# Kernel optimization log

Measured on AMD Instinct MI355X. Metric: run time of the kernel, lower is better.

Reference implementation:

```python
import jax, jax.numpy as jnp
import numpy as np

EPS = 1e-5

def layernorm(x, w, b):
    mu = x.mean(-1, keepdims=True)
    var = x.var(-1, keepdims=True)
    return (x - mu) / jnp.sqrt(var + EPS) * w + b

def silu(x):
    return x * jax.nn.sigmoid(x)

def causal_dwconv(x, w, b):
    # x: (B,L,D), w: (D,K) depthwise causal conv along L
    K = w.shape[1]
    xt = jnp.moveaxis(x, 1, 2)                      # (B,D,L)
    xt = jnp.pad(xt, ((0, 0), (0, 0), (K - 1, 0)))
    y = jax.lax.conv_general_dilated(xt, w[:, None, :], (1,), 'VALID',
        dimension_numbers=('NCH', 'OIH', 'NCH'), feature_group_count=w.shape[0])
    return jnp.moveaxis(y + b[None, :, None], 2, 1)

def mamba_layer(x, p):
    # LayerNorm + Mamba selective scan; returns (out, C) with C the per-step C projection ("C_fast")
    xn = layernorm(x, p['ln_w'], p['ln_b'])
    xz = xn @ p['in_proj_w']                        # (B,L,2*Di)
    Di = p['conv_w'].shape[0]
    xh, z = xz[..., :Di], xz[..., Di:]
    xh = silu(causal_dwconv(xh, p['conv_w'], p['conv_b']))
    dbl = xh @ p['x_proj_w']                        # (B,L,R+2*S)
    R = p['dt_proj_w'].shape[0]
    S = p['A_log'].shape[1]
    dt = jax.nn.softplus(dbl[..., :R] @ p['dt_proj_w'] + p['dt_proj_b'])  # (B,L,Di)
    Bm = dbl[..., R:R + S]                          # (B,L,S)
    Cm = dbl[..., R + S:]                           # (B,L,S)
    A = -jnp.exp(p['A_log'])                        # (Di,S)
    dA = jnp.exp(dt[..., None] * A)                 # (B,L,Di,S)
    dBx = dt[..., None] * Bm[:, :, None, :] * xh[..., None]
    def step(h, inp):
        a, bx = inp
        h = a * h + bx
        return h, h
    h0 = jnp.zeros((x.shape[0], Di, S), x.dtype)
    _, hs = jax.lax.scan(step, h0, (jnp.moveaxis(dA, 1, 0), jnp.moveaxis(dBx, 1, 0)))
    y = jnp.einsum('lbds,bls->bld', hs, Cm) + p['D'] * xh
    y = y * silu(z)
    return y @ p['out_proj_w'], Cm

def run_chunks(x, k, p):
    # contiguous L-chunks folded into batch (chunks are independent sequences)
    B, L, D = x.shape
    y, C = mamba_layer(x.reshape(B * k, L // k, D), p)
    return y.reshape(B, L, D), C.reshape(B, k, L // k, -1)

def batchnorm(h, g, b):
    mu = h.mean((0, 1))
    var = h.var((0, 1))
    return (h - mu) / jnp.sqrt(var + EPS) * g + b

def freq_ffn(x, fc1_w, bn1_g, bn1_b, r_mat, i_mat, rb, ib, fc2_w, bn2_g, bn2_b):
    h = jax.nn.relu(batchnorm(jnp.einsum('bnc,hc->bnh', x, fc1_w), bn1_g, bn1_b))
    xf = jnp.fft.fft(h, axis=1, norm='ortho')
    # torch einsum 'bnc,cc->bnc' multiplies by the DIAGONAL of the matrix
    rd = jnp.diagonal(r_mat)
    idg = jnp.diagonal(i_mat)
    xr = jax.nn.relu(xf.real * rd - xf.imag * idg + rb)
    xi = jax.nn.relu(xf.imag * rd + xf.real * idg + ib)
    h = jnp.fft.ifft(xr + 1j * xi, axis=1, norm='ortho').real.astype(x.dtype)
    return batchnorm(jnp.einsum('bnh,ch->bnc', h, fc2_w), bn2_g, bn2_b)


def setup_inputs() -> dict:
    key = jax.random.key(0)
    B, L, D = 4, 512, 128
    Di, S, R, K, H = 256, 64, 8, 4, 256
    ks = jax.random.split(key, 16)
    rn = lambda k, sh, s=1.0: (jax.random.normal(k, sh) * s).astype(jnp.float32)
    return {
        'x': rn(ks[0], (B, L, D)),
        'ln_w': jnp.ones((D,), jnp.float32), 'ln_b': jnp.zeros((D,), jnp.float32),
        'in_proj_w': rn(ks[1], (D, 2 * Di), D ** -0.5),
        'conv_w': rn(ks[2], (Di, K), 0.3),
        'conv_b': jnp.zeros((Di,), jnp.float32),
        'x_proj_w': rn(ks[3], (Di, R + 2 * S), Di ** -0.5),
        'dt_proj_w': rn(ks[4], (R, Di), R ** -0.5),
        'dt_proj_b': rn(ks[5], (Di,), 0.1) - 4.0,
        'A_log': jnp.log(jnp.tile(jnp.arange(1, S + 1, dtype=jnp.float32), (Di, 1))),
        'D_param': jnp.ones((Di,), jnp.float32),
        'out_proj_w': rn(ks[6], (Di, D), Di ** -0.5),
        'norm1_w': jnp.ones((D,), jnp.float32), 'norm1_b': jnp.zeros((D,), jnp.float32),
        'norm2_w': jnp.ones((D,), jnp.float32), 'norm2_b': jnp.zeros((D,), jnp.float32),
        'fc1_w': rn(ks[7], (H, D), D ** -0.5),
        'bn1_g': jnp.ones((H,), jnp.float32), 'bn1_b': jnp.zeros((H,), jnp.float32),
        'r_mat': rn(ks[8], (H, H), 0.02),
        'i_mat': rn(ks[9], (H, H), 0.02),
        'rb': rn(ks[10], (H,), 0.02),
        'ib': rn(ks[11], (H,), 0.02),
        'fc2_w': rn(ks[12], (D, H), H ** -0.5),
        'bn2_g': jnp.ones((D,), jnp.float32), 'bn2_b': jnp.zeros((D,), jnp.float32),
    }


def reference(x, ln_w, ln_b, in_proj_w, conv_w, conv_b, x_proj_w, dt_proj_w, dt_proj_b,
              A_log, D_param, out_proj_w, norm1_w, norm1_b, norm2_w, norm2_b,
              fc1_w, bn1_g, bn1_b, r_mat, i_mat, rb, ib, fc2_w, bn2_g, bn2_b):
    p = dict(ln_w=ln_w, ln_b=ln_b, in_proj_w=in_proj_w, conv_w=conv_w, conv_b=conv_b,
             x_proj_w=x_proj_w, dt_proj_w=dt_proj_w, dt_proj_b=dt_proj_b,
             A_log=A_log, D=D_param, out_proj_w=out_proj_w)
    x_o, C0 = mamba_layer(x, p)                 # full sequence
    y1, C1 = run_chunks(x, 2, p)                # 2 halves
    y2, C2 = run_chunks(x, 4, p)                # 4 quarters
    y3, C3 = run_chunks(x, 8, p)                # 8 eighths
    x_o = x_o + y1 + y2 + y3                    # drop_path = Identity
    xo = x + layernorm(x_o, norm1_w, norm1_b)
    out = xo + freq_ffn(layernorm(xo, norm2_w, norm2_b),
                        fc1_w, bn1_g, bn1_b, r_mat, i_mat, rb, ib, fc2_w, bn2_g, bn2_b)
    return out, C0, C1, C2, C3
```

## Files before the change

### kernel.cpp

```cpp
#include <hip/hip_runtime.h>
#include <hip/hip_bf16.h>
#include <math.h>


constexpr int NT = 2048;
constexpr int Di = 256;
constexpr float EPSF = 1e-5f;
constexpr float LOG2E = 1.4426950408889634f;
constexpr float ISQ512 = 0.04419417382415922f;

typedef __attribute__((ext_vector_type(8))) short short8;
typedef __attribute__((ext_vector_type(4))) float f32x4;

constexpr long O_CS2B  = 0;
constexpr long O_CSIB  = 262144;
constexpr long O_A2    = 524288;
constexpr long O_FC1B  = 540672;
constexpr long O_FC2B  = 557056;
constexpr long O_INPB  = 573440;
constexpr long O_XPB   = 606208;
constexpr long O_OPB   = 630784;
constexpr long O_RD    = 647168;
constexpr long O_IDG   = 647424;
constexpr long O_XNB   = 647680;
constexpr long O_XZ    = 778752;
constexpr long O_XH    = 1827328;
constexpr long O_DBL   = 3924480;
constexpr long O_DTT   = 5038592;
constexpr long O_YS    = 7135744;
constexpr long O_XO    = 9232896;
constexpr long O_LN2B  = 9495040;
constexpr long O_H1    = 9626112;
constexpr long O_H1NTB = 10150400;
constexpr long O_XRI   = 10412544;
constexpr long O_XRITB = 11461120;
constexpr long O_H2B   = 11985408;
constexpr long O_F2    = 12247552;
constexpr long O_ST1   = 12509696;
constexpr long O_ST2   = 12510208;
constexpr long O_DXT   = O_H1;
constexpr long O_XHB   = O_H1;
constexpr long O_YACCB = O_F2;
constexpr long O_XO1   = O_H2B;

__device__ __forceinline__ ushort bf16bits(float v) {
  __hip_bfloat16 h = __float2bfloat16(v);
  return *(ushort*)&h;
}

__global__ __launch_bounds__(256) void k_tables(
    const float* __restrict__ A_log, const float* __restrict__ fc1_w,
    const float* __restrict__ fc2_w, const float* __restrict__ r_mat,
    const float* __restrict__ i_mat, const float* __restrict__ in_proj_w,
    const float* __restrict__ x_proj_w, const float* __restrict__ out_proj_w,
    float* __restrict__ ws) {
  __shared__ float ct[512];
  int tid = threadIdx.x;
  ct[tid]       = cosf((float)tid * (6.283185307179586f / 512.0f)) * ISQ512;
  ct[tid + 256] = cosf((float)(tid + 256) * (6.283185307179586f / 512.0f)) * ISQ512;
  __syncthreads();
  __hip_bfloat16* cs2b = (__hip_bfloat16*)(ws + O_CS2B);
  __hip_bfloat16* csib = (__hip_bfloat16*)(ws + O_CSIB);
  int i = blockIdx.x * 256 + tid;
  if (i < 524288) {
    int r = i >> 9, n = i & 511;
    float v;
    if (r < 512) v = ct[(r * n) & 511];
    else         v = -ct[((r - 512) * n + 384) & 511];
    cs2b[i] = __float2bfloat16(v);
  } else {
    int j = i - 524288;
    int n = j >> 10, kp = j & 1023;
    float v;
    if (kp < 512) v = ct[(n * kp) & 511];
    else          v = -ct[(n * (kp - 512) + 384) & 511];
    csib[j] = __float2bfloat16(v);
  }
  if (i < 16384) ws[O_A2 + i] = -expf(A_log[i]) * LOG2E;
  if (i < 32768) {
    ((__hip_bfloat16*)(ws + O_FC1B))[i] = __float2bfloat16(fc1_w[i]);
    ((__hip_bfloat16*)(ws + O_FC2B))[i] = __float2bfloat16(fc2_w[i]);
  }
  if (i < 65536) {
    int n = i >> 7, k = i & 127;
    ((__hip_bfloat16*)(ws + O_INPB))[i] = __float2bfloat16(in_proj_w[k * 512 + n]);
  }
  if (i < 49152) {
    int n = i >> 8, k = i & 255;
    float v = (n < 136) ? x_proj_w[k * 136 + n] : 0.f;
    ((__hip_bfloat16*)(ws + O_XPB))[i] = __float2bfloat16(v);
  }
  if (i < 32768 + 0) {}
  if (i >= 65536 && i < 65536 + 32768) {
    int j = i - 65536;
    int n = j >> 8, k = j & 255;
    ((__hip_bfloat16*)(ws + O_OPB))[j] = __float2bfloat16(out_proj_w[k * 128 + n]);
  }
  if (i < 256) {
    ws[O_RD + i] = r_mat[i * 256 + i];
    ws[O_IDG + i] = i_mat[i * 256 + i];
  }
}

__global__ void k_ln1(const float* __restrict__ x, const float* __restrict__ w,
                      const float* __restrict__ b, ushort* __restrict__ outb) {
  int lane = threadIdx.x & 63;
  int t = (blockIdx.x * 256 + threadIdx.x) >> 6;
  float v0 = x[t * 128 + lane], v1 = x[t * 128 + 64 + lane];
  float s = v0 + v1, sq = v0 * v0 + v1 * v1;
#pragma unroll
  for (int off = 32; off; off >>= 1) { s += __shfl_xor(s, off); sq += __shfl_xor(sq, off); }
  float mu = s * (1.f / 128.f);
  float rstd = rsqrtf(sq * (1.f / 128.f) - mu * mu + EPSF);
  outb[t * 128 + lane]      = bf16bits((v0 - mu) * rstd * w[lane] + b[lane]);
  outb[t * 128 + 64 + lane] = bf16bits((v1 - mu) * rstd * w[64 + lane] + b[64 + lane]);
}

__global__ void k_lndbl(const float* __restrict__ x, const float* __restrict__ xo1,
                        const float* __restrict__ w1, const float* __restrict__ b1,
                        const float* __restrict__ w2, const float* __restrict__ b2,
                        float* __restrict__ xo, ushort* __restrict__ ln2b) {
  int lane = threadIdx.x & 63;
  int t = (blockIdx.x * 256 + threadIdx.x) >> 6;
  float u0 = xo1[t * 128 + lane], u1 = xo1[t * 128 + 64 + lane];
  float s = u0 + u1, sq = u0 * u0 + u1 * u1;
#pragma unroll
  for (int off = 32; off; off >>= 1) { s += __shfl_xor(s, off); sq += __shfl_xor(sq, off); }
  float mu = s * (1.f / 128.f);
  float rstd = rsqrtf(sq * (1.f / 128.f) - mu * mu + EPSF);
  float a0 = x[t * 128 + lane]      + (u0 - mu) * rstd * w1[lane] + b1[lane];
  float a1 = x[t * 128 + 64 + lane] + (u1 - mu) * rstd * w1[64 + lane] + b1[64 + lane];
  xo[t * 128 + lane] = a0;
  xo[t * 128 + 64 + lane] = a1;
  s = a0 + a1; sq = a0 * a0 + a1 * a1;
#pragma unroll
  for (int off = 32; off; off >>= 1) { s += __shfl_xor(s, off); sq += __shfl_xor(sq, off); }
  mu = s * (1.f / 128.f);
  rstd = rsqrtf(sq * (1.f / 128.f) - mu * mu + EPSF);
  ln2b[t * 128 + lane]      = bf16bits((a0 - mu) * rstd * w2[lane] + b2[lane]);
  ln2b[t * 128 + 64 + lane] = bf16bits((a1 - mu) * rstd * w2[64 + lane] + b2[64 + lane]);
}

template <bool OUTBF16>
__global__ __launch_bounds__(256) void k_gmfma(const ushort* __restrict__ A,
                                               const ushort* __restrict__ Bt,
                                               void* __restrict__ Cv,
                                               int M, int N, int K,
                                               long sA, long sBt, long sC) {
  A += (long)blockIdx.z * sA;
  Bt += (long)blockIdx.z * sBt;
  int lane = threadIdx.x & 63, wid = threadIdx.x >> 6;
  int m0 = blockIdx.y * 64 + wid * 16, n0 = blockIdx.x * 64;
  const ushort* arow = A + (long)(m0 + (lane & 15)) * K + (lane >> 4) * 8;
  const ushort* brow = Bt + (long)(n0 + (lane & 15)) * K + (lane >> 4) * 8;
  f32x4 acc0 = {0.f, 0.f, 0.f, 0.f}, acc1 = acc0, acc2 = acc0, acc3 = acc0;
#pragma unroll 4
  for (int k0 = 0; k0 < K; k0 += 32) {
    short8 av = *(const short8*)(arow + k0);
    short8 b0 = *(const short8*)(brow + k0);
    short8 b1 = *(const short8*)(brow + 16L * K + k0);
    short8 b2 = *(const short8*)(brow + 32L * K + k0);
    short8 b3 = *(const short8*)(brow + 48L * K + k0);
    acc0 = __builtin_amdgcn_mfma_f32_16x16x32_bf16(av, b0, acc0, 0, 0, 0);
    acc1 = __builtin_amdgcn_mfma_f32_16x16x32_bf16(av, b1, acc1, 0, 0, 0);
    acc2 = __builtin_amdgcn_mfma_f32_16x16x32_bf16(av, b2, acc2, 0, 0, 0);
    acc3 = __builtin_amdgcn_mfma_f32_16x16x32_bf16(av, b3, acc3, 0, 0, 0);
  }
  int r0 = (lane >> 4) * 4, c0 = lane & 15;
#pragma unroll
  for (int j = 0; j < 4; ++j) {
    long row = m0 + r0 + j;
    float v[4] = {acc0[j], acc1[j], acc2[j], acc3[j]};
    if (OUTBF16) {
      __hip_bfloat16* C = (__hip_bfloat16*)Cv + blockIdx.z * sC;
#pragma unroll
      for (int c = 0; c < 4; ++c) {
        int n = n0 + c * 16 + c0;
        if (n < N) C[row * N + n] = __float2bfloat16(v[c]);
      }
    } else {
      float* C = (float*)Cv + blockIdx.z * sC;
#pragma unroll
      for (int c = 0; c < 4; ++c) {
        int n = n0 + c * 16 + c0;
        if (n < N) C[row * N + n] = v[c];
      }
    }
  }
}

__global__ void k_conv4(const float* __restrict__ xz, const float* __restrict__ cw,
                        const float* __restrict__ cb, float* __restrict__ xh,
                        ushort* __restrict__ xhb) {
  int i = blockIdx.x * 256 + threadIdx.x;
  int t = i >> 8, d = i & 255;
  float w0 = cw[d * 4 + 0], w1 = cw[d * 4 + 1], w2 = cw[d * 4 + 2], w3 = cw[d * 4 + 3];
  float bias = cb[d];
  float x0  = xz[(long)t * 512 + d];
  float xm1 = t >= 1 ? xz[(long)(t - 1) * 512 + d] : 0.f;
  float xm2 = t >= 2 ? xz[(long)(t - 2) * 512 + d] : 0.f;
  float xm3 = t >= 3 ? xz[(long)(t - 3) * 512 + d] : 0.f;
  if ((t & 63) >= 3) {
    float s = fmaf(w0, xm3, fmaf(w1, xm2, fmaf(w2, xm1, fmaf(w3, x0, bias))));
    float sil = s / (1.f + expf(-s));
    ushort sb = bf16bits(sil);
#pragma unroll
    for (int v = 0; v < 4; ++v) { xh[v * 524288 + i] = sil; xhb[v * 524288 + i] = sb; }
  } else {
#pragma unroll
    for (int v = 0; v < 4; ++v) {
      int lv = t & ((512 >> v) - 1);
      float s = fmaf(w3, x0, bias);
      if (lv >= 1) s = fmaf(w2, xm1, s);
      if (lv >= 2) s = fmaf(w1, xm2, s);
      if (lv >= 3) s = fmaf(w0, xm3, s);
      float sil = s / (1.f + expf(-s));
      xh[v * 524288 + i] = sil;
      xhb[v * 524288 + i] = bf16bits(sil);
    }
  }
}

__global__ __launch_bounds__(256) void k_dtx(const float* __restrict__ dbl,
                                             const float* __restrict__ xh,
                                             const float* __restrict__ w,
                                             const float* __restrict__ bias,
                                             float* __restrict__ DTT,
                                             float* __restrict__ DXT,
                                             float* __restrict__ outC) {
  __shared__ float r8T[8][64];
  __shared__ float xt[64][65];
  __shared__ float wt[8][64];
  int v = blockIdx.z, t0 = blockIdx.y * 64, d0 = blockIdx.x * 64;
  int j = threadIdx.x;
  if (j < 128) {
    int t = j >> 1, half = j & 1;
    float4 q = *(const float4*)&dbl[((long)v * NT + t0 + t) * 136 + half * 4];
    r8T[half * 4 + 0][t] = q.x; r8T[half * 4 + 1][t] = q.y;
    r8T[half * 4 + 2][t] = q.z; r8T[half * 4 + 3][t] = q.w;
  } else {
    int idx = j - 128;
    int r = idx >> 4, dl4 = (idx & 15) * 4;
    float4 q = *(const float4*)&w[r * 256 + d0 + dl4];
    wt[r][dl4] = q.x; wt[r][dl4 + 1] = q.y; wt[r][dl4 + 2] = q.z; wt[r][dl4 + 3] = q.w;
  }
#pragma unroll
  for (int it = 0; it < 4; ++it) {
    int row = (j >> 4) + it * 16, col4 = (j & 15) * 4;
    float4 q = *(const float4*)&xh[((long)v * NT + t0 + row) * 256 + d0 + col4];
    xt[row][col4] = q.x; xt[row][col4 + 1] = q.y;
    xt[row][col4 + 2] = q.z; xt[row][col4 + 3] = q.w;
  }
  __syncthreads();
  int lane = j & 63, w4 = j >> 6;
#pragma unroll
  for (int k = 0; k < 16; ++k) {
    int dl = w4 * 16 + k, d = d0 + dl;
    float s = bias[d];
#pragma unroll
    for (int r = 0; r < 8; ++r) s = fmaf(r8T[r][lane], wt[r][dl], s);
    float dtv = fmaxf(s, 0.f) + log1pf(expf(-fabsf(s)));
    float dx = dtv * xt[lane][dl];
    long oi = ((long)(v * 256 + d)) * 2048 + t0 + lane;
    DTT[oi] = dtv;
    DXT[oi] = dx;
  }
  if (blockIdx.x == 0) {
#pragma unroll
    for (int k2 = 0; k2 < 16; ++k2) {
      int idx = k2 * 256 + j;
      int tl = idx >> 6, s2 = idx & 63;
      outC[(long)v * 131072 + (long)(t0 + tl) * 64 + s2] =
          dbl[((long)v * NT + t0 + tl) * 136 + 72 + s2];
    }
  }
}

template <int CTRL>
__device__ __forceinline__ float dpp_add(float x) {
  int t = __builtin_amdgcn_update_dpp(0, __float_as_int(x), CTRL, 0xF, 0xF, true);
  return x + __int_as_float(t);
}

__global__ __launch_bounds__(256) void k_scan(const float* __restrict__ DTT,
                                              const float* __restrict__ DXT,
                                              const float* __restrict__ dbl,
                                              const float* __restrict__ A2,
                                              float* __restrict__ ys) {
  int lane = threadIdx.x & 63;
  int gwid = (blockIdx.x * 256 + threadIdx.x) >> 6;
  int v, base;
  if (gwid < 1024)      { v = 0; base = 0; }
  else if (gwid < 3072) { v = 1; base = 1024; }
  else if (gwid < 7168) { v = 2; base = 3072; }
  else                  { v = 3; base = 7168; }
  int local = gwid - base;
  int b = local >> 8, d = local & 255;
  int Lp = 512 >> v;
  int t0 = b * Lp;
  const float* dtrow = DTT + ((long)(v * 256 + d)) * 2048 + t0;
  const float* dxrow = DXT + ((long)(v * 256 + d)) * 2048 + t0;
  const float* dblp = dbl + ((long)v * NT + t0) * 136;
  float* ysp = ys + (long)v * NT * Di + (long)((b << 8) + d) * Lp;
  float a2 = A2[d * 64 + lane];
  float h = 0.f;

#define LOADG(BB, CC, G)                                                     \
  _Pragma("unroll") for (int q = 0; q < 8; ++q) {                            \
    BB[q] = rowp[((G) * 8 + q) * 136 + 8 + lane];                            \
    CC[q] = rowp[((G) * 8 + q) * 136 + 72 + lane];                           \
  }
#define PROCG(BB, CC, G)                                                     \
  _Pragma("unroll") for (int q = 0; q < 8; ++q) {                            \
    int l2 = (G) * 8 + q;                                                    \
    float sdt = __int_as_float(__builtin_amdgcn_readlane(__float_as_int(rdt), l2)); \
    float sdx = __int_as_float(__builtin_amdgcn_readlane(__float_as_int(rdx), l2)); \
    float a = __builtin_amdgcn_exp2f(sdt * a2);                              \
    h = fmaf(a, h, sdx * BB[q]);                                             \
    float p = h * CC[q];                                                     \
    p = dpp_add<0x111>(p); p = dpp_add<0x112>(p);                            \
    p = dpp_add<0x114>(p); p = dpp_add<0x118>(p);                            \
    p = dpp_add<0x142>(p); p = dpp_add<0x143>(p);                            \
    float tot = __int_as_float(__builtin_amdgcn_readlane(__float_as_int(p), 63)); \
    if (lane == l2) ybuf = tot;                                              \
  }

  for (int c = 0; c < Lp; c += 64) {
    float rdt = dtrow[c + lane];
    float rdx = dxrow[c + lane];
    const float* rowp = dblp + (long)c * 136;
    float ybuf = 0.f;
    float b0[8], c0[8], b1[8], c1[8];
    LOADG(b0, c0, 0)
    LOADG(b1, c1, 1)
    PROCG(b0, c0, 0) LOADG(b0, c0, 2)
    PROCG(b1, c1, 1) LOADG(b1, c1, 3)
    PROCG(b0, c0, 2) LOADG(b0, c0, 4)
    PROCG(b1, c1, 3) LOADG(b1, c1, 5)
    PROCG(b0, c0, 4) LOADG(b0, c0, 6)
    PROCG(b1, c1, 5) LOADG(b1, c1, 7)
    PROCG(b0, c0, 6)
    PROCG(b1, c1, 7)
    ysp[c + lane] = ybuf;
  }
#undef LOADG
#undef PROCG
}

__global__ void k_yfull(const float* __restrict__ ys, const float* __restrict__ xh,
                        const float* __restrict__ xz, const float* __restrict__ Dp,
                        ushort* __restrict__ yaccb) {
  int i = blockIdx.x * 256 + threadIdx.x;
  int t = i >> 8, d = i & 255;
  float z = xz[(long)t * 512 + 256 + d];
  float sil = z / (1.f + expf(-z));
  float Dd = Dp[d];
  float s = 0.f;
#pragma unroll
  for (int v = 0; v < 4; ++v) {
    int Lp = 512 >> v;
    int b = t >> (9 - v);
    int l = t & (Lp - 1);
    float ysv = ys[(long)v * NT * Di + (long)((b << 8) + d) * Lp + l];
    float xhv = xh[(long)v * NT * Di + i];
    s += ysv + Dd * xhv;
  }
  yaccb[i] = bf16bits(s * sil);
}

__global__ __launch_bounds__(256) void k_bnstats(const float* __restrict__ h, int F,
                                                 const float* __restrict__ g,
                                                 const float* __restrict__ b,
                                                 float* __restrict__ scale,
                                                 float* __restrict__ shift) {
  int f = blockIdx.x;
  float s = 0.f, sq = 0.f;
  for (int t = threadIdx.x; t < NT; t += 256) {
    float v = h[(long)t * F + f];
    s += v; sq += v * v;
  }
#pragma unroll
  for (int off = 32; off; off >>= 1) { s += __shfl_xor(s, off); sq += __shfl_xor(sq, off); }
  __shared__ float red[2][4];
  int w = threadIdx.x >> 6;
  if ((threadIdx.x & 63) == 0) { red[0][w] = s; red[1][w] = sq; }
  __syncthreads();
  if (threadIdx.x == 0) {
    s = red[0][0] + red[0][1] + red[0][2] + red[0][3];
    sq = red[1][0] + red[1][1] + red[1][2] + red[1][3];
    float mu = s * (1.f / NT);
    float var = sq * (1.f / NT) - mu * mu;
    float sc = g[f] * rsqrtf(var + EPSF);
    scale[f] = sc;
    shift[f] = b[f] - mu * sc;
  }
}

__global__ __launch_bounds__(256) void k_bnreluT(const float* __restrict__ h1,
                                                 const float* __restrict__ scale,
                                                 const float* __restrict__ shift,
                                                 ushort* __restrict__ outT) {
  __shared__ float tile[64][65];
  int t0 = blockIdx.x * 64, f0 = blockIdx.y * 64, b = blockIdx.z;
  int tid = threadIdx.x;
#pragma unroll
  for (int i = 0; i < 16; ++i) {
    int idx = i * 256 + tid;
    int r = idx >> 6, c = idx & 63;
    int f = f0 + c;
    float v = h1[((long)(b * 512 + t0 + r)) * 256 + f];
    tile[r][c] = fmaxf(fmaf(v, scale[f], shift[f]), 0.f);
  }
  __syncthreads();
  int tc2 = (tid & 31) * 2, fr0 = tid >> 5;
#pragma unroll
  for (int i = 0; i < 8; ++i) {
    int fr = fr0 + i * 8;
    uint u = ((uint)bf16bits(tile[tc2 + 1][fr]) << 16) | bf16bits(tile[tc2][fr]);
    long off = (long)b * 131072 + (long)(f0 + fr) * 512 + t0 + tc2;
    *(uint*)(outT + off) = u;
  }
}

__global__ __launch_bounds__(256) void k_freqT(const float* __restrict__ XRI,
                                               const float* __restrict__ rd,
                                               const float* __restrict__ idg,
                                               const float* __restrict__ rb,
                                               const float* __restrict__ ib,
                                               ushort* __restrict__ outT) {
  __shared__ float tr[64][65], ti[64][65];
  int n0 = blockIdx.x * 64, f0 = blockIdx.y * 64, b = blockIdx.z;
  int tid = threadIdx.x;
#pragma unroll
  for (int i = 0; i < 16; ++i) {
    int idx = i * 256 + tid;
    int r = idx >> 6, c = idx & 63;
    int f = f0 + c;
    long base = (long)b * 262144 + (long)(n0 + r) * 256 + f;
    float a = XRI[base], b2 = XRI[base + 131072];
    tr[r][c] = fmaxf(a * rd[f] - b2 * idg[f] + rb[f], 0.f);
    ti[r][c] = fmaxf(b2 * rd[f] + a * idg[f] + ib[f], 0.f);
  }
  __syncthreads();
  int tc2 = (tid & 31) * 2, fr0 = tid >> 5;
#pragma unroll
  for (int i = 0; i < 8; ++i) {
    int fr = fr0 + i * 8;
    long offr = (long)b * 262144 + (long)(f0 + fr) * 1024 + n0 + tc2;
    uint ur = ((uint)bf16bits(tr[tc2 + 1][fr]) << 16) | bf16bits(tr[tc2][fr]);
    uint ui = ((uint)bf16bits(ti[tc2 + 1][fr]) << 16) | bf16bits(ti[tc2][fr]);
    *(uint*)(outT + offr) = ur;
    *(uint*)(outT + offr + 512) = ui;
  }
}

__global__ void k_final(const float* __restrict__ xo, const float* __restrict__ f2,
                        const float* __restrict__ scale, const float* __restrict__ shift,
                        float* __restrict__ out) {
  int i = blockIdx.x * 256 + threadIdx.x;
  int c = i & 127;
  out[i] = xo[i] + fmaf(f2[i], scale[c], shift[c]);
}

extern "C" void kernel_launch(void* const* d_in, const int* in_sizes, int n_in,
                              void* d_out, int out_size, void* d_ws, size_t ws_size,
                              hipStream_t stream) {
  const float* x         = (const float*)d_in[0];
  const float* ln_w      = (const float*)d_in[1];
  const float* ln_b      = (const float*)d_in[2];
  const float* in_proj_w = (const float*)d_in[3];
  const float* conv_w    = (const float*)d_in[4];
  const float* conv_b    = (const float*)d_in[5];
  const float* x_proj_w  = (const float*)d_in[6];
  const float* dt_proj_w = (const float*)d_in[7];
  const float* dt_proj_b = (const float*)d_in[8];
  const float* A_log     = (const float*)d_in[9];
  const float* D_param   = (const float*)d_in[10];
  const float* out_proj_w= (const float*)d_in[11];
  const float* n1w       = (const float*)d_in[12];
  const float* n1b       = (const float*)d_in[13];
  const float* n2w       = (const float*)d_in[14];
  const float* n2b       = (const float*)d_in[15];
  const float* fc1_w     = (const float*)d_in[16];
  const float* bn1_g     = (const float*)d_in[17];
  const float* bn1_b     = (const float*)d_in[18];
  const float* r_mat     = (const float*)d_in[19];
  const float* i_mat     = (const float*)d_in[20];
  const float* rb        = (const float*)d_in[21];
  const float* ib        = (const float*)d_in[22];
  const float* fc2_w     = (const float*)d_in[23];
  const float* bn2_g     = (const float*)d_in[24];
  const float* bn2_b     = (const float*)d_in[25];
  float* ws  = (float*)d_ws;
  float* out = (float*)d_out;

  k_tables<<<4096, 256, 0, stream>>>(A_log, fc1_w, fc2_w, r_mat, i_mat,
                                     in_proj_w, x_proj_w, out_proj_w, ws);
  k_ln1<<<512, 256, 0, stream>>>(x, ln_w, ln_b, (ushort*)(ws + O_XNB));
  k_gmfma<false><<<dim3(8, 32, 1), 256, 0, stream>>>(
      (const ushort*)(ws + O_XNB), (const ushort*)(ws + O_INPB), ws + O_XZ,
      2048, 512, 128, 0, 0, 0);
  k_conv4<<<2048, 256, 0, stream>>>(ws + O_XZ, conv_w, conv_b, ws + O_XH,
                                    (ushort*)(ws + O_XHB));
  k_gmfma<false><<<dim3(3, 32, 4), 256, 0, stream>>>(
      (const ushort*)(ws + O_XHB), (const ushort*)(ws + O_XPB), ws + O_DBL,
      2048, 136, 256, 524288L, 0, 278528L);
  k_dtx<<<dim3(4, 32, 4), 256, 0, stream>>>(ws + O_DBL, ws + O_XH, dt_proj_w,
                                            dt_proj_b, ws + O_DTT, ws + O_DXT,
                                            out + 262144);
  k_scan<<<3840, 256, 0, stream>>>(ws + O_DTT, ws + O_DXT, ws + O_DBL,
                                   ws + O_A2, ws + O_YS);
  k_yfull<<<2048, 256, 0, stream>>>(ws + O_YS, ws + O_XH, ws + O_XZ, D_param,
                                    (ushort*)(ws + O_YACCB));
  k_gmfma<false><<<dim3(2, 32, 1), 256, 0, stream>>>(
      (const ushort*)(ws + O_YACCB), (const ushort*)(ws + O_OPB), ws + O_XO1,
      2048, 128, 256, 0, 0, 0);
  k_lndbl<<<512, 256, 0, stream>>>(x, ws + O_XO1, n1w, n1b, n2w, n2b,
                                   ws + O_XO, (ushort*)(ws + O_LN2B));
  k_gmfma<false><<<dim3(4, 32, 1), 256, 0, stream>>>(
      (const ushort*)(ws + O_LN2B), (const ushort*)(ws + O_FC1B), ws + O_H1,
      2048, 256, 128, 0, 0, 0);
  k_bnstats<<<256, 256, 0, stream>>>(ws + O_H1, 256, bn1_g, bn1_b,
                                     ws + O_ST1, ws + O_ST1 + 256);
  k_bnreluT<<<dim3(8, 4, 4), 256, 0, stream>>>(ws + O_H1, ws + O_ST1,
                                               ws + O_ST1 + 256,
                                               (ushort*)(ws + O_H1NTB));
  k_gmfma<false><<<dim3(4, 16, 4), 256, 0, stream>>>(
      (const ushort*)(ws + O_CS2B), (const ushort*)(ws + O_H1NTB), ws + O_XRI,
      1024, 256, 512, 0, 131072L, 262144L);
  k_freqT<<<dim3(8, 4, 4), 256, 0, stream>>>(ws + O_XRI, ws + O_RD, ws + O_IDG,
                                             rb, ib, (ushort*)(ws + O_XRITB));
  k_gmfma<true><<<dim3(4, 8, 4), 256, 0, stream>>>(
      (const ushort*)(ws + O_CSIB), (const ushort*)(ws + O_XRITB), ws + O_H2B,
      512, 256, 1024, 0, 262144L, 131072L);
  k_gmfma<false><<<dim3(2, 32, 1), 256, 0, stream>>>(
      (const ushort*)(ws + O_H2B), (const ushort*)(ws + O_FC2B), ws + O_F2,
      2048, 128, 256, 0, 0, 0);
  k_bnstats<<<128, 256, 0, stream>>>(ws + O_F2, 128, bn2_g, bn2_b,
                                     ws + O_ST2, ws + O_ST2 + 128);
  k_final<<<1024, 256, 0, stream>>>(ws + O_XO, ws + O_F2, ws + O_ST2,
                                    ws + O_ST2 + 128, out);
}
```

Measured before the change: 297.5 us.

## Store xz/xh intermediates in bf16, fuse LN1 into tables, atomic BN stats

```diff
diff --git a/kernel.cpp b/kernel.cpp
--- a/kernel.cpp
+++ b/kernel.cpp
@@ -23,8 +23,8 @@
 constexpr long O_RD    = 647168;
 constexpr long O_IDG   = 647424;
 constexpr long O_XNB   = 647680;
-constexpr long O_XZ    = 778752;
-constexpr long O_XH    = 1827328;
+constexpr long O_XZB   = 778752;
+constexpr long O_XHB   = 1827328;
 constexpr long O_DBL   = 3924480;
 constexpr long O_DTT   = 5038592;
 constexpr long O_YS    = 7135744;
@@ -36,16 +36,18 @@
 constexpr long O_XRITB = 11461120;
 constexpr long O_H2B   = 11985408;
 constexpr long O_F2    = 12247552;
-constexpr long O_ST1   = 12509696;
-constexpr long O_ST2   = 12510208;
+constexpr long O_SQ1   = 12509696;
+constexpr long O_SQ2   = 12510208;
 constexpr long O_DXT   = O_H1;
-constexpr long O_XHB   = O_H1;
 constexpr long O_YACCB = O_F2;
 constexpr long O_XO1   = O_H2B;
 
 __device__ __forceinline__ ushort bf16bits(float v) {
   __hip_bfloat16 h = __float2bfloat16(v);
   return *(ushort*)&h;
+}
+__device__ __forceinline__ float bfu(ushort u) {
+  return __uint_as_float((uint)u << 16);
 }
 
 __global__ __launch_bounds__(256) void k_tables(
@@ -53,7 +55,8 @@
     const float* __restrict__ fc2_w, const float* __restrict__ r_mat,
     const float* __restrict__ i_mat, const float* __restrict__ in_proj_w,
     const float* __restrict__ x_proj_w, const float* __restrict__ out_proj_w,
-    float* __restrict__ ws) {
+    const float* __restrict__ x, const float* __restrict__ ln_w,
+    const float* __restrict__ ln_b, float* __restrict__ ws) {
   __shared__ float ct[512];
   int tid = threadIdx.x;
   ct[tid]       = cosf((float)tid * (6.283185307179586f / 512.0f)) * ISQ512;
@@ -90,8 +93,7 @@
     float v = (n < 136) ? x_proj_w[k * 136 + n] : 0.f;
     ((__hip_bfloat16*)(ws + O_XPB))[i] = __float2bfloat16(v);
   }
-  if (i < 32768 + 0) {}
-  if (i >= 65536 && i < 65536 + 32768) {
+  if (i >= 65536 && i < 98304) {
     int j = i - 65536;
     int n = j >> 8, k = j & 255;
     ((__hip_bfloat16*)(ws + O_OPB))[j] = __float2bfloat16(out_proj_w[k * 128 + n]);
@@ -100,20 +102,21 @@
     ws[O_RD + i] = r_mat[i * 256 + i];
     ws[O_IDG + i] = i_mat[i * 256 + i];
   }
-}
-
-__global__ void k_ln1(const float* __restrict__ x, const float* __restrict__ w,
-                      const float* __restrict__ b, ushort* __restrict__ outb) {
-  int lane = threadIdx.x & 63;
-  int t = (blockIdx.x * 256 + threadIdx.x) >> 6;
-  float v0 = x[t * 128 + lane], v1 = x[t * 128 + 64 + lane];
-  float s = v0 + v1, sq = v0 * v0 + v1 * v1;
-#pragma unroll
-  for (int off = 32; off; off >>= 1) { s += __shfl_xor(s, off); sq += __shfl_xor(sq, off); }
-  float mu = s * (1.f / 128.f);
-  float rstd = rsqrtf(sq * (1.f / 128.f) - mu * mu + EPSF);
-  outb[t * 128 + lane]      = bf16bits((v0 - mu) * rstd * w[lane] + b[lane]);
-  outb[t * 128 + 64 + lane] = bf16bits((v1 - mu) * rstd * w[64 + lane] + b[64 + lane]);
+  if (i < 512) ws[O_SQ1 + i] = 0.f;
+  if (i < 256) ws[O_SQ2 + i] = 0.f;
+  if (blockIdx.x < 512) {
+    ushort* outb = (ushort*)(ws + O_XNB);
+    int lane = tid & 63;
+    int t = (blockIdx.x * 256 + tid) >> 6;
+    float v0 = x[t * 128 + lane], v1 = x[t * 128 + 64 + lane];
+    float s = v0 + v1, sq = v0 * v0 + v1 * v1;
+#pragma unroll
+    for (int off = 32; off; off >>= 1) { s += __shfl_xor(s, off); sq += __shfl_xor(sq, off); }
+    float mu = s * (1.f / 128.f);
+    float rstd = rsqrtf(sq * (1.f / 128.f) - mu * mu + EPSF);
+    outb[t * 128 + lane]      = bf16bits((v0 - mu) * rstd * ln_w[lane] + ln_b[lane]);
+    outb[t * 128 + 64 + lane] = bf16bits((v1 - mu) * rstd * ln_w[64 + lane] + ln_b[64 + lane]);
+  }
 }
 
 __global__ void k_lndbl(const float* __restrict__ x, const float* __restrict__ xo1,
@@ -189,23 +192,22 @@
   }
 }
 
-__global__ void k_conv4(const float* __restrict__ xz, const float* __restrict__ cw,
-                        const float* __restrict__ cb, float* __restrict__ xh,
-                        ushort* __restrict__ xhb) {
+__global__ void k_conv4(const ushort* __restrict__ xzb, const float* __restrict__ cw,
+                        const float* __restrict__ cb, ushort* __restrict__ xhb) {
   int i = blockIdx.x * 256 + threadIdx.x;
   int t = i >> 8, d = i & 255;
   float w0 = cw[d * 4 + 0], w1 = cw[d * 4 + 1], w2 = cw[d * 4 + 2], w3 = cw[d * 4 + 3];
   float bias = cb[d];
-  float x0  = xz[(long)t * 512 + d];
-  float xm1 = t >= 1 ? xz[(long)(t - 1) * 512 + d] : 0.f;
-  float xm2 = t >= 2 ? xz[(long)(t - 2) * 512 + d] : 0.f;
-  float xm3 = t >= 3 ? xz[(long)(t - 3) * 512 + d] : 0.f;
+  float x0  = bfu(xzb[(long)t * 512 + d]);
+  float xm1 = t >= 1 ? bfu(xzb[(long)(t - 1) * 512 + d]) : 0.f;
+  float xm2 = t >= 2 ? bfu(xzb[(long)(t - 2) * 512 + d]) : 0.f;
+  float xm3 = t >= 3 ? bfu(xzb[(long)(t - 3) * 512 + d]) : 0.f;
   if ((t & 63) >= 3) {
     float s = fmaf(w0, xm3, fmaf(w1, xm2, fmaf(w2, xm1, fmaf(w3, x0, bias))));
     float sil = s / (1.f + expf(-s));
     ushort sb = bf16bits(sil);
 #pragma unroll
-    for (int v = 0; v < 4; ++v) { xh[v * 524288 + i] = sil; xhb[v * 524288 + i] = sb; }
+    for (int v = 0; v < 4; ++v) xhb[v * 524288 + i] = sb;
   } else {
 #pragma unroll
     for (int v = 0; v < 4; ++v) {
@@ -215,14 +217,13 @@
       if (lv >= 2) s = fmaf(w1, xm2, s);
       if (lv >= 3) s = fmaf(w0, xm3, s);
       float sil = s / (1.f + expf(-s));
-      xh[v * 524288 + i] = sil;
       xhb[v * 524288 + i] = bf16bits(sil);
     }
   }
 }
 
 __global__ __launch_bounds__(256) void k_dtx(const float* __restrict__ dbl,
-                                             const float* __restrict__ xh,
+                                             const ushort* __restrict__ xhb,
                                              const float* __restrict__ w,
                                              const float* __restrict__ bias,
                                              float* __restrict__ DTT,
@@ -247,9 +248,11 @@
 #pragma unroll
   for (int it = 0; it < 4; ++it) {
     int row = (j >> 4) + it * 16, col4 = (j & 15) * 4;
-    float4 q = *(const float4*)&xh[((long)v * NT + t0 + row) * 256 + d0 + col4];
-    xt[row][col4] = q.x; xt[row][col4 + 1] = q.y;
-    xt[row][col4 + 2] = q.z; xt[row][col4 + 3] = q.w;
+    uint2 u = *(const uint2*)&xhb[((long)v * NT + t0 + row) * 256 + d0 + col4];
+    xt[row][col4 + 0] = __uint_as_float(u.x << 16);
+    xt[row][col4 + 1] = __uint_as_float(u.x & 0xffff0000u);
+    xt[row][col4 + 2] = __uint_as_float(u.y << 16);
+    xt[row][col4 + 3] = __uint_as_float(u.y & 0xffff0000u);
   }
   __syncthreads();
   int lane = j & 63, w4 = j >> 6;
@@ -347,12 +350,12 @@
 #undef PROCG
 }
 
-__global__ void k_yfull(const float* __restrict__ ys, const float* __restrict__ xh,
-                        const float* __restrict__ xz, const float* __restrict__ Dp,
+__global__ void k_yfull(const float* __restrict__ ys, const ushort* __restrict__ xhb,
+                        const ushort* __restrict__ xzb, const float* __restrict__ Dp,
                         ushort* __restrict__ yaccb) {
   int i = blockIdx.x * 256 + threadIdx.x;
   int t = i >> 8, d = i & 255;
-  float z = xz[(long)t * 512 + 256 + d];
+  float z = bfu(xzb[(long)t * 512 + 256 + d]);
   float sil = z / (1.f + expf(-z));
   float Dd = Dp[d];
   float s = 0.f;
@@ -362,54 +365,54 @@
     int b = t >> (9 - v);
     int l = t & (Lp - 1);
     float ysv = ys[(long)v * NT * Di + (long)((b << 8) + d) * Lp + l];
-    float xhv = xh[(long)v * NT * Di + i];
+    float xhv = bfu(xhb[(long)v * 524288 + i]);
     s += ysv + Dd * xhv;
   }
   yaccb[i] = bf16bits(s * sil);
 }
 
-__global__ __launch_bounds__(256) void k_bnstats(const float* __restrict__ h, int F,
+template <int F>
+__global__ __launch_bounds__(256) void k_bnpart(const float* __restrict__ h,
+                                                float* __restrict__ SQ) {
+  constexpr int NREP = 256 / F;
+  constexpr int TPR = 32 / NREP;
+  int tid = threadIdx.x;
+  int f = tid & (F - 1), rep = tid / F;
+  int t0 = blockIdx.x * 32 + rep * TPR;
+  float s = 0.f, q = 0.f;
+#pragma unroll
+  for (int tt = 0; tt < TPR; ++tt) {
+    float v = h[(long)(t0 + tt) * F + f];
+    s += v; q += v * v;
+  }
+  atomicAdd(&SQ[f], s);
+  atomicAdd(&SQ[F + f], q);
+}
+
+__global__ __launch_bounds__(256) void k_bnreluT(const float* __restrict__ h1,
+                                                 const float* __restrict__ SQ,
                                                  const float* __restrict__ g,
-                                                 const float* __restrict__ b,
-                                                 float* __restrict__ scale,
-                                                 float* __restrict__ shift) {
-  int f = blockIdx.x;
-  float s = 0.f, sq = 0.f;
-  for (int t = threadIdx.x; t < NT; t += 256) {
-    float v = h[(long)t * F + f];
-    s += v; sq += v * v;
-  }
-#pragma unroll
-  for (int off = 32; off; off >>= 1) { s += __shfl_xor(s, off); sq += __shfl_xor(sq, off); }
-  __shared__ float red[2][4];
-  int w = threadIdx.x >> 6;
-  if ((threadIdx.x & 63) == 0) { red[0][w] = s; red[1][w] = sq; }
-  __syncthreads();
-  if (threadIdx.x == 0) {
-    s = red[0][0] + red[0][1] + red[0][2] + red[0][3];
-    sq = red[1][0] + red[1][1] + red[1][2] + red[1][3];
-    float mu = s * (1.f / NT);
-    float var = sq * (1.f / NT) - mu * mu;
-    float sc = g[f] * rsqrtf(var + EPSF);
-    scale[f] = sc;
-    shift[f] = b[f] - mu * sc;
-  }
-}
-
-__global__ __launch_bounds__(256) void k_bnreluT(const float* __restrict__ h1,
-                                                 const float* __restrict__ scale,
-                                                 const float* __restrict__ shift,
+                                                 const float* __restrict__ bb,
                                                  ushort* __restrict__ outT) {
   __shared__ float tile[64][65];
+  __shared__ float sc_s[64], sh_s[64];
   int t0 = blockIdx.x * 64, f0 = blockIdx.y * 64, b = blockIdx.z;
   int tid = threadIdx.x;
+  if (tid < 64) {
+    int f = f0 + tid;
+    float mu = SQ[f] * (1.f / NT);
+    float var = SQ[256 + f] * (1.f / NT) - mu * mu;
+    float sc = g[f] * rsqrtf(var + EPSF);
+    sc_s[tid] = sc;
+    sh_s[tid] = bb[f] - mu * sc;
+  }
+  __syncthreads();
 #pragma unroll
   for (int i = 0; i < 16; ++i) {
     int idx = i * 256 + tid;
     int r = idx >> 6, c = idx & 63;
-    int f = f0 + c;
-    float v = h1[((long)(b * 512 + t0 + r)) * 256 + f];
-    tile[r][c] = fmaxf(fmaf(v, scale[f], shift[f]), 0.f);
+    float v = h1[((long)(b * 512 + t0 + r)) * 256 + f0 + c];
+    tile[r][c] = fmaxf(fmaf(v, sc_s[c], sh_s[c]), 0.f);
   }
   __syncthreads();
   int tc2 = (tid & 31) * 2, fr0 = tid >> 5;
@@ -454,12 +457,25 @@
   }
 }
 
-__global__ void k_final(const float* __restrict__ xo, const float* __restrict__ f2,
-                        const float* __restrict__ scale, const float* __restrict__ shift,
-                        float* __restrict__ out) {
-  int i = blockIdx.x * 256 + threadIdx.x;
+__global__ __launch_bounds__(256) void k_final(const float* __restrict__ xo,
+                                               const float* __restrict__ f2,
+                                               const float* __restrict__ SQ,
+                                               const float* __restrict__ g,
+                                               const float* __restrict__ bb,
+                                               float* __restrict__ out) {
+  __shared__ float sc_s[128], sh_s[128];
+  int tid = threadIdx.x;
+  if (tid < 128) {
+    float mu = SQ[tid] * (1.f / NT);
+    float var = SQ[128 + tid] * (1.f / NT) - mu * mu;
+    float sc = g[tid] * rsqrtf(var + EPSF);
+    sc_s[tid] = sc;
+    sh_s[tid] = bb[tid] - mu * sc;
+  }
+  __syncthreads();
+  int i = blockIdx.x * 256 + tid;
   int c = i & 127;
-  out[i] = xo[i] + fmaf(f2[i], scale[c], shift[c]);
+  out[i] = xo[i] + fmaf(f2[i], sc_s[c], sh_s[c]);
 }
 
 extern "C" void kernel_launch(void* const* d_in, const int* in_sizes, int n_in,
@@ -495,22 +511,23 @@
   float* out = (float*)d_out;
 
   k_tables<<<4096, 256, 0, stream>>>(A_log, fc1_w, fc2_w, r_mat, i_mat,
-                                     in_proj_w, x_proj_w, out_proj_w, ws);
-  k_ln1<<<512, 256, 0, stream>>>(x, ln_w, ln_b, (ushort*)(ws + O_XNB));
-  k_gmfma<false><<<dim3(8, 32, 1), 256, 0, stream>>>(
-      (const ushort*)(ws + O_XNB), (const ushort*)(ws + O_INPB), ws + O_XZ,
+                                     in_proj_w, x_proj_w, out_proj_w,
+                                     x, ln_w, ln_b, ws);
+  k_gmfma<true><<<dim3(8, 32, 1), 256, 0, stream>>>(
+      (const ushort*)(ws + O_XNB), (const ushort*)(ws + O_INPB), ws + O_XZB,
       2048, 512, 128, 0, 0, 0);
-  k_conv4<<<2048, 256, 0, stream>>>(ws + O_XZ, conv_w, conv_b, ws + O_XH,
+  k_conv4<<<2048, 256, 0, stream>>>((const ushort*)(ws + O_XZB), conv_w, conv_b,
                                     (ushort*)(ws + O_XHB));
   k_gmfma<false><<<dim3(3, 32, 4), 256, 0, stream>>>(
       (const ushort*)(ws + O_XHB), (const ushort*)(ws + O_XPB), ws + O_DBL,
       2048, 136, 256, 524288L, 0, 278528L);
-  k_dtx<<<dim3(4, 32, 4), 256, 0, stream>>>(ws + O_DBL, ws + O_XH, dt_proj_w,
-                                            dt_proj_b, ws + O_DTT, ws + O_DXT,
-                                            out + 262144);
+  k_dtx<<<dim3(4, 32, 4), 256, 0, stream>>>(ws + O_DBL, (const ushort*)(ws + O_XHB),
+                                            dt_proj_w, dt_proj_b, ws + O_DTT,
+                                            ws + O_DXT, out + 262144);
   k_scan<<<3840, 256, 0, stream>>>(ws + O_DTT, ws + O_DXT, ws + O_DBL,
                                    ws + O_A2, ws + O_YS);
-  k_yfull<<<2048, 256, 0, stream>>>(ws + O_YS, ws + O_XH, ws + O_XZ, D_param,
+  k_yfull<<<2048, 256, 0, stream>>>(ws + O_YS, (const ushort*)(ws + O_XHB),
+                                    (const ushort*)(ws + O_XZB), D_param,
                                     (ushort*)(ws + O_YACCB));
   k_gmfma<false><<<dim3(2, 32, 1), 256, 0, stream>>>(
       (const ushort*)(ws + O_YACCB), (const ushort*)(ws + O_OPB), ws + O_XO1,
@@ -520,11 +537,9 @@
   k_gmfma<false><<<dim3(4, 32, 1), 256, 0, stream>>>(
       (const ushort*)(ws + O_LN2B), (const ushort*)(ws + O_FC1B), ws + O_H1,
       2048, 256, 128, 0, 0, 0);
-  k_bnstats<<<256, 256, 0, stream>>>(ws + O_H1, 256, bn1_g, bn1_b,
-                                     ws + O_ST1, ws + O_ST1 + 256);
-  k_bnreluT<<<dim3(8, 4, 4), 256, 0, stream>>>(ws + O_H1, ws + O_ST1,
-                                               ws + O_ST1 + 256,
-                                               (ushort*)(ws + O_H1NTB));
+  k_bnpart<256><<<64, 256, 0, stream>>>(ws + O_H1, ws + O_SQ1);
+  k_bnreluT<<<dim3(8, 4, 4), 256, 0, stream>>>(ws + O_H1, ws + O_SQ1, bn1_g,
+                                               bn1_b, (ushort*)(ws + O_H1NTB));
   k_gmfma<false><<<dim3(4, 16, 4), 256, 0, stream>>>(
       (const ushort*)(ws + O_CS2B), (const ushort*)(ws + O_H1NTB), ws + O_XRI,
       1024, 256, 512, 0, 131072L, 262144L);
@@ -536,8 +551,7 @@
   k_gmfma<false><<<dim3(2, 32, 1), 256, 0, stream>>>(
       (const ushort*)(ws + O_H2B), (const ushort*)(ws + O_FC2B), ws + O_F2,
       2048, 128, 256, 0, 0, 0);
-  k_bnstats<<<128, 256, 0, stream>>>(ws + O_F2, 128, bn2_g, bn2_b,
-                                     ws + O_ST2, ws + O_ST2 + 128);
-  k_final<<<1024, 256, 0, stream>>>(ws + O_XO, ws + O_F2, ws + O_ST2,
-                                    ws + O_ST2 + 128, out);
-}
+  k_bnpart<128><<<64, 256, 0, stream>>>(ws + O_F2, ws + O_SQ2);
+  k_final<<<1024, 256, 0, stream>>>(ws + O_XO, ws + O_F2, ws + O_SQ2,
+                                    bn2_g, bn2_b, out);
+}
```

Result: no change. 292.7 us (-1.6%).
